# Kernel tuning notes

Hardware: AMD Instinct MI355X
Metric: run time of the kernel (lower is better)

## Reference

```python
import jax, jax.numpy as jnp
import numpy as np


def _causal_mask(n):
    # pixelSNAIL get_causal_mask: strict lower triangular (pixel i attends to pixels < i)
    return jnp.tril(jnp.ones((n, n), dtype=jnp.float32), k=-1)


def setup_inputs() -> dict:
    key = jax.random.key(0)
    kq, kk, kv = jax.random.split(key, 3)
    B, H, W, C, CM = 32, 32, 32, 128, 256
    return {
        "query": jax.random.normal(kq, (B, H, W, C), dtype=jnp.float32),
        "key": jax.random.normal(kk, (B, H, W, C), dtype=jnp.float32),
        "value": jax.random.normal(kv, (B, H, W, CM), dtype=jnp.float32),
    }


def reference(query, key, value):
    B = query.shape[0]
    C = key.shape[-1]
    CM = value.shape[-1]
    Nk = int(np.prod(key.shape[1:-1]))
    Nq = int(np.prod(query.shape[1:-1]))
    q = query.reshape(B, Nq, C)
    k = key.reshape(B, Nk, C)
    v = value.reshape(B, Nk, CM)
    # raw QK^T (no 1/sqrt(d) scaling in original)
    dot = jnp.einsum('bqc,bkc->bqk', q, k)
    # NON-STANDARD: softmax over full row first, then multiply by strict causal mask
    probs = jax.nn.softmax(dot, axis=-1) * _causal_mask(Nq)[None]
    mixed = jnp.einsum('bqk,bkm->bqm', probs, v)
    return mixed.reshape(query.shape[:-1] + (CM,))
```

## Files before the change

### kernel.cpp

```cpp
#include <hip/hip_runtime.h>


typedef __attribute__((ext_vector_type(8))) short short8;
typedef __attribute__((ext_vector_type(4))) float floatx4;

#define MFMA16(a, b, c) __builtin_amdgcn_mfma_f32_16x16x32_bf16((a), (b), (c), 0, 0, 0)

constexpr int N = 1024, C = 128, CM = 256, BATCH = 32;
constexpr int BM = 64;
constexpr int BN = 32;
constexpr int NT = N / BN;
constexpr int KFRAG = BN * C;
constexpr int VFRAG = BN * CM;
constexpr int PSTR = 40;

__device__ __forceinline__ unsigned short f2bf(float x) {
    unsigned int u = __float_as_uint(x);
    u += 0x7fffu + ((u >> 16) & 1u);
    return (unsigned short)(u >> 16);
}
__device__ __forceinline__ float bf2f(unsigned short h) {
    return __uint_as_float(((unsigned int)h) << 16);
}
__device__ __forceinline__ uint4 pack8(const unsigned short* s) {
    uint4 u;
    u.x = (unsigned)s[0] | ((unsigned)s[1] << 16);
    u.y = (unsigned)s[2] | ((unsigned)s[3] << 16);
    u.z = (unsigned)s[4] | ((unsigned)s[5] << 16);
    u.w = (unsigned)s[6] | ((unsigned)s[7] << 16);
    return u;
}
__device__ __forceinline__ uint2 pack4(const unsigned short* s) {
    uint2 u;
    u.x = (unsigned)s[0] | ((unsigned)s[1] << 16);
    u.y = (unsigned)s[2] | ((unsigned)s[3] << 16);
    return u;
}
__device__ __forceinline__ void gl2lds16(const unsigned short* g, unsigned short* l) {
    __builtin_amdgcn_global_load_lds(
        (const __attribute__((address_space(1))) void*)g,
        (__attribute__((address_space(3))) void*)l, 16, 0, 0);
}

__global__ __launch_bounds__(256, 4)
void prep_kernel(const float* __restrict__ kg, const float* __restrict__ vg,
                 unsigned short* __restrict__ khi, unsigned short* __restrict__ klo,
                 unsigned short* __restrict__ vf)
{
    __shared__ __align__(16) unsigned short sKh[KFRAG];
    __shared__ __align__(16) unsigned short sKl[KFRAG];
    __shared__ __align__(16) unsigned short sV[VFRAG];

    const int tid = threadIdx.x;
    const int l = tid & 63, w = tid >> 6;
    const int tile = blockIdx.x, bat = blockIdx.y;
    const int n0 = tile * BN;
    const float* kb = kg + ((size_t)bat * N + n0) * C;
    const float* vb = vg + ((size_t)bat * N + n0) * CM;

#pragma unroll
    for (int it = 0; it < 4; ++it) {
        const int lin = tid + it * 256;
        const float4 x = *(const float4*)(kb + (size_t)lin * 4);
        const int cr = lin >> 1, h = lin & 1;
        const int slot = cr ^ ((cr >> 4) & 7);
        float xs[4] = {x.x, x.y, x.z, x.w};
        unsigned short hi[4], lo[4];
#pragma unroll
        for (int e = 0; e < 4; ++e) {
            unsigned short hb = f2bf(xs[e]);
            hi[e] = hb;
            lo[e] = f2bf(xs[e] - bf2f(hb));
        }
        *(uint2*)(&sKh[slot * 8 + h * 4]) = pack4(hi);
        *(uint2*)(&sKl[slot * 8 + h * 4]) = pack4(lo);
    }

#pragma unroll
    for (int g = 0; g < 2; ++g) {
        const int k0 = g * 16 + w * 4;
        float xa[4][4];
#pragma unroll
        for (int d = 0; d < 4; ++d) {
            const float4 t = *(const float4*)(vb + (size_t)(k0 + d) * CM + l * 4);
            xa[0][d] = t.x; xa[1][d] = t.y; xa[2][d] = t.z; xa[3][d] = t.w;
        }
        const int qq = k0 >> 3, j0 = k0 & 7;
#pragma unroll
        for (int e = 0; e < 4; ++e) {
            const int cm = l * 4 + e;
            const int ct = cm >> 4, rr = cm & 15;
            const int ch = ct * 64 + qq * 16 + rr;
            const int slot = ch ^ ((ch >> 6) & 15);
            unsigned short o[4];
#pragma unroll
            for (int d = 0; d < 4; ++d) o[d] = f2bf(xa[e][d]);
            *(uint2*)(&sV[slot * 8 + j0]) = pack4(o);
        }
    }

    __syncthreads();

    unsigned short* khb = khi + ((size_t)bat * NT + tile) * KFRAG;
    unsigned short* klb = klo + ((size_t)bat * NT + tile) * KFRAG;
    unsigned short* vfb = vf + ((size_t)bat * NT + tile) * VFRAG;

#pragma unroll
    for (int it = 0; it < 2; ++it) {
        const int oc = tid + it * 256;
        const int cr = ((oc & 15) + ((oc >> 8) << 4)) * 16 + ((oc >> 6) & 3) * 4 + ((oc >> 4) & 3);
        const int slot = cr ^ ((cr >> 4) & 7);
        *(uint4*)(khb + (size_t)oc * 8) = *(const uint4*)(&sKh[slot * 8]);
        *(uint4*)(klb + (size_t)oc * 8) = *(const uint4*)(&sKl[slot * 8]);
    }
#pragma unroll
    for (int it = 0; it < 4; ++it) {
        const int oc = tid + it * 256;
        const int slot = oc ^ ((oc >> 6) & 15);
        *(uint4*)(vfb + (size_t)oc * 8) = *(const uint4*)(&sV[slot * 8]);
    }
}

__global__ __launch_bounds__(256, 2)
void attn_kernel(const float* __restrict__ qg, float* __restrict__ og,
                 const unsigned short* __restrict__ khi,
                 const unsigned short* __restrict__ klo,
                 const unsigned short* __restrict__ vf)
{
    __shared__ __align__(16) unsigned short sKhi[2][KFRAG];
    __shared__ __align__(16) unsigned short sKlo[2][KFRAG];
    __shared__ __align__(16) unsigned short sV[VFRAG];
    __shared__ __align__(16) unsigned short sP[4 * 16 * PSTR];

    const int tid = threadIdx.x;
    const int w = tid >> 6, ln = tid & 63;
    const int r = ln & 15, qd = ln >> 4;
    const int bat = blockIdx.x;
    const int qt = blockIdx.y;
    const int q0 = qt * BM;

    const float* qb = qg + (size_t)bat * N * C;
    float* ob = og + (size_t)bat * N * CM;
    const unsigned short* khb = khi + (size_t)bat * NT * KFRAG;
    const unsigned short* klb = klo + (size_t)bat * NT * KFRAG;
    const unsigned short* vfb = vf + (size_t)bat * NT * VFRAG;

    short8 qhi[4], qlo[4];
    {
        const float* qr = qb + (size_t)(q0 + w * 16 + r) * C + qd * 8;
#pragma unroll
        for (int ks = 0; ks < 4; ++ks) {
            float4 a = *(const float4*)(qr + ks * 32);
            float4 b = *(const float4*)(qr + ks * 32 + 4);
            float xs[8] = {a.x, a.y, a.z, a.w, b.x, b.y, b.z, b.w};
            short8 h, l;
#pragma unroll
            for (int j = 0; j < 8; ++j) {
                unsigned short hb = f2bf(xs[j]);
                h[j] = (short)hb;
                l[j] = (short)f2bf(xs[j] - bf2f(hb));
            }
            qhi[ks] = h;
            qlo[ks] = l;
        }
    }

    floatx4 oacc[16];
#pragma unroll
    for (int ct = 0; ct < 16; ++ct) oacc[ct] = (floatx4){0.f, 0.f, 0.f, 0.f};
    float lsum[4] = {0.f, 0.f, 0.f, 0.f};
    const int irow = q0 + w * 16 + qd * 4;
    unsigned short* wP = &sP[w * 16 * PSTR];

    gl2lds16(khb + (size_t)tid * 8,         &sKhi[0][tid * 8]);
    gl2lds16(khb + (size_t)(tid + 256) * 8, &sKhi[0][(tid + 256) * 8]);
    gl2lds16(klb + (size_t)tid * 8,         &sKlo[0][tid * 8]);
    gl2lds16(klb + (size_t)(tid + 256) * 8, &sKlo[0][(tid + 256) * 8]);

    for (int tile = 0; tile < NT; ++tile) {
        const bool pvt = (tile <= 2 * qt + 1);
        const int cb = tile & 1;

        if (pvt) {
            const unsigned short* vs = vfb + (size_t)tile * VFRAG;
#pragma unroll
            for (int i = 0; i < 4; ++i)
                gl2lds16(vs + (size_t)(tid + i * 256) * 8, &sV[(tid + i * 256) * 8]);
        }
        if (tile + 1 < NT) {
            const unsigned short* k1 = khb + (size_t)(tile + 1) * KFRAG;
            const unsigned short* l1 = klb + (size_t)(tile + 1) * KFRAG;
            unsigned short* dh = &sKhi[cb ^ 1][0];
            unsigned short* dl = &sKlo[cb ^ 1][0];
            gl2lds16(k1 + (size_t)tid * 8,         dh + tid * 8);
            gl2lds16(k1 + (size_t)(tid + 256) * 8, dh + (tid + 256) * 8);
            gl2lds16(l1 + (size_t)tid * 8,         dl + tid * 8);
            gl2lds16(l1 + (size_t)(tid + 256) * 8, dl + (tid + 256) * 8);
            asm volatile("s_waitcnt vmcnt(4)" ::: "memory");
        } else {
            asm volatile("s_waitcnt vmcnt(0)" ::: "memory");
        }
        asm volatile("s_barrier" ::: "memory");

#pragma unroll
        for (int t = 0; t < 2; ++t) {
            floatx4 a0 = (floatx4){0.f, 0.f, 0.f, 0.f};
            floatx4 a1 = (floatx4){0.f, 0.f, 0.f, 0.f};
            floatx4 a2 = (floatx4){0.f, 0.f, 0.f, 0.f};
#pragma unroll
            for (int ks = 0; ks < 4; ++ks) {
                short8 bh = *(const short8*)(&sKhi[cb][(((t * 4 + ks) * 64) + ln) * 8]);
                short8 bl = *(const short8*)(&sKlo[cb][(((t * 4 + ks) * 64) + ln) * 8]);
                a0 = MFMA16(qhi[ks], bh, a0);
                a1 = MFMA16(qlo[ks], bh, a1);
                a2 = MFMA16(qhi[ks], bl, a2);
            }
            const int jglob = tile * BN + t * 16 + r;
#pragma unroll
            for (int rg = 0; rg < 4; ++rg) {
                float s = a0[rg] + a1[rg] + a2[rg];
                float p = __expf(s - 40.0f);
                lsum[rg] += p;
                if (pvt) {
                    float pm = (jglob < irow + rg) ? p : 0.0f;
                    wP[(qd * 4 + rg) * PSTR + t * 16 + r] = f2bf(pm);
                }
            }
        }

        if (pvt) {
            asm volatile("s_waitcnt lgkmcnt(0)" ::: "memory");
            short8 ap = *(const short8*)(&wP[r * PSTR + qd * 8]);
#pragma unroll
            for (int ct = 0; ct < 16; ++ct) {
                short8 bv = *(const short8*)(&sV[(ct * 64 + ln) * 8]);
                oacc[ct] = MFMA16(ap, bv, oacc[ct]);
            }
        }
        asm volatile("s_barrier" ::: "memory");
    }

#pragma unroll
    for (int rg = 0; rg < 4; ++rg) {
        float v = lsum[rg];
        v += __shfl_xor(v, 1);
        v += __shfl_xor(v, 2);
        v += __shfl_xor(v, 4);
        v += __shfl_xor(v, 8);
        lsum[rg] = v;
    }

#pragma unroll
    for (int rg = 0; rg < 4; ++rg) {
        float inv = 1.0f / lsum[rg];
        float* orow = ob + (size_t)(q0 + w * 16 + qd * 4 + rg) * CM;
#pragma unroll
        for (int ct = 0; ct < 16; ++ct)
            orow[ct * 16 + r] = oacc[ct][rg] * inv;
    }
}

extern "C" void kernel_launch(void* const* d_in, const int* in_sizes, int n_in,
                              void* d_out, int out_size, void* d_ws, size_t ws_size,
                              hipStream_t stream) {
    const float* q = (const float*)d_in[0];
    const float* k = (const float*)d_in[1];
    const float* v = (const float*)d_in[2];
    float* o = (float*)d_out;
    (void)n_in; (void)in_sizes; (void)out_size; (void)ws_size;

    unsigned short* khi = (unsigned short*)d_ws;
    unsigned short* klo = khi + (size_t)BATCH * NT * KFRAG;
    unsigned short* vf  = klo + (size_t)BATCH * NT * KFRAG;

    prep_kernel<<<dim3(NT, BATCH), dim3(256), 0, stream>>>(k, v, khi, klo, vf);
    attn_kernel<<<dim3(BATCH, N / BM), dim3(256), 0, stream>>>(q, o, khi, klo, vf);
}
```

Baseline: 159.6 us.

## Double-buffer V tiles and build P operand in registers via permlane swaps

V tiles are now double-buffered in LDS and prefetched one tile ahead alongside K, so the V load no longer stalls the PV MFMA of the current tile. The QK^T MFMA operands are swapped to produce S transposed, which lets each lane convert its probabilities to packed bf16 and rearrange them with permlane32/16 swaps straight into the A-operand layout for PV. This removes the LDS round trip and wait for the P staging buffer. The row-sum reduction changes to match the transposed layout, and LDS usage grows by one extra V buffer, which may affect occupancy.

```diff
diff --git a/kernel.cpp b/kernel.cpp
--- a/kernel.cpp
+++ b/kernel.cpp
@@ -12,7 +12,6 @@
 constexpr int NT = N / BN;
 constexpr int KFRAG = BN * C;
 constexpr int VFRAG = BN * CM;
-constexpr int PSTR = 40;
 
 __device__ __forceinline__ unsigned short f2bf(float x) {
     unsigned int u = __float_as_uint(x);
@@ -21,14 +20,6 @@
 }
 __device__ __forceinline__ float bf2f(unsigned short h) {
     return __uint_as_float(((unsigned int)h) << 16);
-}
-__device__ __forceinline__ uint4 pack8(const unsigned short* s) {
-    uint4 u;
-    u.x = (unsigned)s[0] | ((unsigned)s[1] << 16);
-    u.y = (unsigned)s[2] | ((unsigned)s[3] << 16);
-    u.z = (unsigned)s[4] | ((unsigned)s[5] << 16);
-    u.w = (unsigned)s[6] | ((unsigned)s[7] << 16);
-    return u;
 }
 __device__ __forceinline__ uint2 pack4(const unsigned short* s) {
     uint2 u;
@@ -129,8 +120,7 @@
 {
     __shared__ __align__(16) unsigned short sKhi[2][KFRAG];
     __shared__ __align__(16) unsigned short sKlo[2][KFRAG];
-    __shared__ __align__(16) unsigned short sV[VFRAG];
-    __shared__ __align__(16) unsigned short sP[4 * 16 * PSTR];
+    __shared__ __align__(16) unsigned short sV[2][VFRAG];
 
     const int tid = threadIdx.x;
     const int w = tid >> 6, ln = tid & 63;
@@ -168,25 +158,21 @@
     floatx4 oacc[16];
 #pragma unroll
     for (int ct = 0; ct < 16; ++ct) oacc[ct] = (floatx4){0.f, 0.f, 0.f, 0.f};
-    float lsum[4] = {0.f, 0.f, 0.f, 0.f};
-    const int irow = q0 + w * 16 + qd * 4;
-    unsigned short* wP = &sP[w * 16 * PSTR];
+    float lsum = 0.f;
+    const int qrow = q0 + w * 16 + r;
 
     gl2lds16(khb + (size_t)tid * 8,         &sKhi[0][tid * 8]);
     gl2lds16(khb + (size_t)(tid + 256) * 8, &sKhi[0][(tid + 256) * 8]);
     gl2lds16(klb + (size_t)tid * 8,         &sKlo[0][tid * 8]);
     gl2lds16(klb + (size_t)(tid + 256) * 8, &sKlo[0][(tid + 256) * 8]);
+#pragma unroll
+    for (int i = 0; i < 4; ++i)
+        gl2lds16(vfb + (size_t)(tid + i * 256) * 8, &sV[0][(tid + i * 256) * 8]);
 
     for (int tile = 0; tile < NT; ++tile) {
         const bool pvt = (tile <= 2 * qt + 1);
         const int cb = tile & 1;
 
-        if (pvt) {
-            const unsigned short* vs = vfb + (size_t)tile * VFRAG;
-#pragma unroll
-            for (int i = 0; i < 4; ++i)
-                gl2lds16(vs + (size_t)(tid + i * 256) * 8, &sV[(tid + i * 256) * 8]);
-        }
         if (tile + 1 < NT) {
             const unsigned short* k1 = khb + (size_t)(tile + 1) * KFRAG;
             const unsigned short* l1 = klb + (size_t)(tile + 1) * KFRAG;
@@ -196,12 +182,22 @@
             gl2lds16(k1 + (size_t)(tid + 256) * 8, dh + (tid + 256) * 8);
             gl2lds16(l1 + (size_t)tid * 8,         dl + tid * 8);
             gl2lds16(l1 + (size_t)(tid + 256) * 8, dl + (tid + 256) * 8);
-            asm volatile("s_waitcnt vmcnt(4)" ::: "memory");
+            if (tile + 1 <= 2 * qt + 1) {
+                const unsigned short* vs = vfb + (size_t)(tile + 1) * VFRAG;
+                unsigned short* dv = &sV[cb ^ 1][0];
+#pragma unroll
+                for (int i = 0; i < 4; ++i)
+                    gl2lds16(vs + (size_t)(tid + i * 256) * 8, dv + (tid + i * 256) * 8);
+                asm volatile("s_waitcnt vmcnt(8)" ::: "memory");
+            } else {
+                asm volatile("s_waitcnt vmcnt(4)" ::: "memory");
+            }
         } else {
             asm volatile("s_waitcnt vmcnt(0)" ::: "memory");
         }
         asm volatile("s_barrier" ::: "memory");
 
+        float pk[8];
 #pragma unroll
         for (int t = 0; t < 2; ++t) {
             floatx4 a0 = (floatx4){0.f, 0.f, 0.f, 0.f};
@@ -211,48 +207,48 @@
             for (int ks = 0; ks < 4; ++ks) {
                 short8 bh = *(const short8*)(&sKhi[cb][(((t * 4 + ks) * 64) + ln) * 8]);
                 short8 bl = *(const short8*)(&sKlo[cb][(((t * 4 + ks) * 64) + ln) * 8]);
-                a0 = MFMA16(qhi[ks], bh, a0);
-                a1 = MFMA16(qlo[ks], bh, a1);
-                a2 = MFMA16(qhi[ks], bl, a2);
-            }
-            const int jglob = tile * BN + t * 16 + r;
+                a0 = MFMA16(bh, qhi[ks], a0);
+                a1 = MFMA16(bh, qlo[ks], a1);
+                a2 = MFMA16(bl, qhi[ks], a2);
+            }
+            const int kbase = tile * BN + t * 16 + qd * 4;
 #pragma unroll
             for (int rg = 0; rg < 4; ++rg) {
                 float s = a0[rg] + a1[rg] + a2[rg];
                 float p = __expf(s - 40.0f);
-                lsum[rg] += p;
-                if (pvt) {
-                    float pm = (jglob < irow + rg) ? p : 0.0f;
-                    wP[(qd * 4 + rg) * PSTR + t * 16 + r] = f2bf(pm);
-                }
+                lsum += p;
+                pk[t * 4 + rg] = (kbase + rg < qrow) ? p : 0.0f;
             }
         }
 
         if (pvt) {
-            asm volatile("s_waitcnt lgkmcnt(0)" ::: "memory");
-            short8 ap = *(const short8*)(&wP[r * PSTR + qd * 8]);
+            unsigned int w0, w1, w2, w3;
+            asm("v_cvt_pk_bf16_f32 %0, %1, %2" : "=v"(w0) : "v"(pk[0]), "v"(pk[1]));
+            asm("v_cvt_pk_bf16_f32 %0, %1, %2" : "=v"(w1) : "v"(pk[2]), "v"(pk[3]));
+            asm("v_cvt_pk_bf16_f32 %0, %1, %2" : "=v"(w2) : "v"(pk[4]), "v"(pk[5]));
+            asm("v_cvt_pk_bf16_f32 %0, %1, %2" : "=v"(w3) : "v"(pk[6]), "v"(pk[7]));
+            asm("v_permlane32_swap_b32 %0, %1" : "+v"(w0), "+v"(w2));
+            asm("v_permlane16_swap_b32 %0, %1" : "+v"(w0), "+v"(w2));
+            asm("v_permlane32_swap_b32 %0, %1" : "+v"(w1), "+v"(w3));
+            asm("v_permlane16_swap_b32 %0, %1" : "+v"(w1), "+v"(w3));
+            uint4 apu = make_uint4(w0, w1, w2, w3);
+            short8 ap = *(const short8*)&apu;
 #pragma unroll
             for (int ct = 0; ct < 16; ++ct) {
-                short8 bv = *(const short8*)(&sV[(ct * 64 + ln) * 8]);
+                short8 bv = *(const short8*)(&sV[cb][(ct * 64 + ln) * 8]);
                 oacc[ct] = MFMA16(ap, bv, oacc[ct]);
             }
         }
         asm volatile("s_barrier" ::: "memory");
     }
 
+    float vtot = lsum;
+    vtot += __shfl_xor(vtot, 16);
+    vtot += __shfl_xor(vtot, 32);
+
 #pragma unroll
     for (int rg = 0; rg < 4; ++rg) {
-        float v = lsum[rg];
-        v += __shfl_xor(v, 1);
-        v += __shfl_xor(v, 2);
-        v += __shfl_xor(v, 4);
-        v += __shfl_xor(v, 8);
-        lsum[rg] = v;
-    }
-
-#pragma unroll
-    for (int rg = 0; rg < 4; ++rg) {
-        float inv = 1.0f / lsum[rg];
+        float inv = 1.0f / __shfl(vtot, qd * 4 + rg);
         float* orow = ob + (size_t)(q0 + w * 16 + qd * 4 + rg) * CM;
 #pragma unroll
         for (int ct = 0; ct < 16; ++ct)
```

Result: faster. 151.6 us (-5.0%).
